# Kernel optimization log

Measured on AMD Instinct MI355X. Metric: run time of the kernel, lower is better.

The kernel has to match this reference:

```python
import jax, jax.numpy as jnp
import numpy as np
import math

INPUT_DIM, HIDDEN, OUT_DIM, NUM_LAYERS = 128, 512, 128, 2
GRID_SIZE, ORDER = 5, 3  # efficient-KAN defaults
NBASIS = GRID_SIZE + ORDER  # 8 basis functions per input feature


def _grid():
    h = 2.0 / GRID_SIZE  # grid_range [-1, 1]
    return jnp.asarray(np.arange(-ORDER, GRID_SIZE + ORDER + 1) * h - 1.0, dtype=jnp.float32)  # [12]


def b_splines(x, grid):
    # x: [B, In] -> [B, In, NBASIS] via Cox-de Boor recursion (order 3)
    x = x[..., None]
    bases = ((x >= grid[:-1]) & (x < grid[1:])).astype(x.dtype)
    for p in range(1, ORDER + 1):
        left = (x - grid[:-(p + 1)]) / (grid[p:-1] - grid[:-(p + 1)]) * bases[..., :-1]
        right = (grid[p + 1:] - x) / (grid[p + 1:] - grid[1:-p]) * bases[..., 1:]
        bases = left + right
    return bases


def kan_layer(x, base_w, spline_w, grid):
    # efficient-KAN: silu base branch + B-spline branch
    B = x.shape[0]
    out = jax.nn.silu(x) @ base_w.T
    spl = b_splines(x, grid).reshape(B, -1) @ spline_w.reshape(spline_w.shape[0], -1).T
    return out + spl


def lstm_cell(inp, h, c, w_ih, w_hh, b_ih, b_hh, kan_base, kan_spline, grid):
    gates = inp @ w_ih.T + b_ih + h @ w_hh.T + b_hh  # [B, 3H]
    i_g, f_g, o_g = jnp.split(jax.nn.sigmoid(gates), 3, axis=1)
    g = kan_layer(jnp.concatenate([inp, h], axis=1), kan_base, kan_spline, grid)
    c_next = f_g * c + i_g * g
    h_next = o_g * jnp.tanh(c_next)
    return h_next, c_next


def setup_inputs() -> dict:
    key = jax.random.key(0)
    ks = jax.random.split(key, 32)
    stdv = 1.0 / math.sqrt(HIDDEN)
    u = lambda k, shape: jax.random.uniform(k, shape, jnp.float32, -stdv, stdv)
    d = {"x": jax.random.normal(ks[0], (64, 256, INPUT_DIM), jnp.float32)}
    for L in range(NUM_LAYERS):
        In = INPUT_DIM if L == 0 else HIDDEN
        b = 8 * L
        d[f"w_ih{L}"] = u(ks[b + 1], (3 * HIDDEN, In))
        d[f"w_hh{L}"] = u(ks[b + 2], (3 * HIDDEN, HIDDEN))
        d[f"b_ih{L}"] = jnp.zeros((3 * HIDDEN,), jnp.float32)
        d[f"b_hh{L}"] = jnp.zeros((3 * HIDDEN,), jnp.float32)
        d[f"kan_base{L}"] = u(ks[b + 3], (HIDDEN, In + HIDDEN))
        d[f"kan_spline{L}"] = u(ks[b + 4], (HIDDEN, In + HIDDEN, NBASIS)) * 0.1
    d["fc_w"] = u(ks[20], (OUT_DIM, HIDDEN))
    d["fc_b"] = u(ks[21], (OUT_DIM,))
    return d


def reference(x, w_ih0, w_hh0, b_ih0, b_hh0, kan_base0, kan_spline0,
              w_ih1, w_hh1, b_ih1, b_hh1, kan_base1, kan_spline1, fc_w, fc_b):
    grid = _grid()
    B = x.shape[0]
    layers = [
        (w_ih0, w_hh0, b_ih0, b_hh0, kan_base0, kan_spline0),
        (w_ih1, w_hh1, b_ih1, b_hh1, kan_base1, kan_spline1),
    ]
    h0 = tuple(jnp.zeros((B, HIDDEN), x.dtype) for _ in range(NUM_LAYERS))
    c0 = tuple(jnp.zeros((B, HIDDEN), x.dtype) for _ in range(NUM_LAYERS))

    def step(carry, x_t):
        hs, cs = carry
        hs, cs = list(hs), list(cs)
        inp = x_t
        for L in range(NUM_LAYERS):
            w_ih, w_hh, b_ih, b_hh, kb, ksw = layers[L]
            hs[L], cs[L] = lstm_cell(inp, hs[L], cs[L], w_ih, w_hh, b_ih, b_hh, kb, ksw, grid)
            inp = hs[L]
        return (tuple(hs), tuple(cs)), None

    xs = jnp.swapaxes(x, 0, 1)  # [T, B, D]
    (hs, _), _ = jax.lax.scan(step, (h0, c0), xs)
    return hs[-1] @ fc_w.T + fc_b
```

## Files before the change

### kernel.cpp

```cpp
#include <hip/hip_runtime.h>
#include <math.h>
#include <stdint.h>

namespace {

typedef __attribute__((ext_vector_type(8))) short short8v;
typedef __attribute__((ext_vector_type(4))) float f32x4;

constexpr int TT = 256;

constexpr size_t OFF_ST = 0;
constexpr size_t OFF_P0 = 98304;
constexpr size_t OFF_P1 = 884736;
constexpr size_t OFF_WF = 1671168;
constexpr size_t OFF_FF = 11894784;
constexpr size_t WS_NEED = 12959744ull * 4;

constexpr size_t WFLO = 10223616;
constexpr size_t FFLO = 1064960;
constexpr size_t FLB1 = 409600;

__device__ __forceinline__ float sigmoidf_(float v) { return 1.0f / (1.0f + expf(-v)); }

__device__ __forceinline__ ushort bf16h(float v) {
    uint32_t u = __float_as_uint(v);
    return (ushort)((u + 0x7fffu + ((u >> 16) & 1u)) >> 16);
}
__device__ __forceinline__ float bf16f(ushort h) { return __uint_as_float(((uint32_t)h) << 16); }

__device__ __forceinline__ void bspline8(float x, float* out) {
    const float KG[12] = {-2.2f,-1.8f,-1.4f,-1.0f,-0.6f,-0.2f,
                           0.2f, 0.6f, 1.0f, 1.4f, 1.8f, 2.2f};
    float b[11];
#pragma unroll
    for (int i = 0; i < 11; ++i)
        b[i] = (x >= KG[i] && x < KG[i + 1]) ? 1.0f : 0.0f;
#pragma unroll
    for (int p = 1; p <= 3; ++p) {
#pragma unroll
        for (int i = 0; i + p < 11; ++i) {
            float l = (x - KG[i])         * (1.0f / (KG[i + p] - KG[i]));
            float r = (KG[i + p + 1] - x) * (1.0f / (KG[i + p + 1] - KG[i + 1]));
            b[i] = l * b[i] + r * b[i + 1];
        }
    }
#pragma unroll
    for (int i = 0; i < 8; ++i) out[i] = b[i];
}

__device__ __forceinline__ void putFeat(int l, int k, int b, float z,
                                        ushort* __restrict__ fe)
{
    const int NSL = l ? 16 : 10, KC = l ? 512 : 320;
    const int kh = (k >= KC) ? 1 : 0, kr = k - kh * KC;
    const int sl = kr >> 5, kg = (kr >> 3) & 3, j = kr & 7;
    const size_t cell = (size_t)((b >> 4) * 64 + (b & 15) + 16 * kg) * 8 + j;
    const size_t LB = l ? FLB1 : 0;
    const size_t slb = ((size_t)kh * NSL + sl) * 2048 + cell;
    const size_t pstep = (size_t)2 * NSL * 2048;

    auto putp = [&](int p, float v) {
        size_t idx = LB + (size_t)p * pstep + slb;
        ushort h = bf16h(v);
        fe[idx] = h;
        fe[FFLO + idx] = bf16h(v - bf16f(h));
    };
    putp(0, z);
    putp(1, z / (1.0f + expf(-z)));
    float bs[8];
    bspline8(z, bs);
#pragma unroll
    for (int r = 0; r < 8; ++r) putp(2 + r, bs[r]);
}

__global__ __launch_bounds__(256) void sentinel_kernel(float* out, float v) {
    int i = blockIdx.x * 256 + threadIdx.x;
    if (i < 8192) out[i] = v;
}

__global__ __launch_bounds__(256) void wbuild_kernel(
    ushort* __restrict__ wf,
    const float* __restrict__ w_ih0, const float* __restrict__ w_hh0,
    const float* __restrict__ kb0, const float* __restrict__ ksp0,
    const float* __restrict__ w_ih1, const float* __restrict__ w_hh1,
    const float* __restrict__ kb1, const float* __restrict__ ksp1)
{
    const int gid = blockIdx.x * 256 + threadIdx.x;
    const int s = gid >> 6, lane = gid & 63;
    int wid, sl;
    if (s < 7680) { wid = s / 10; sl = s % 10; }
    else          { wid = 768 + (s - 7680) / 16; sl = (s - 7680) % 16; }
    const int l = wid >= 768 ? 1 : 0;
    const int r2 = wid - l * 768;
    const int kh = r2 >= 384 ? 1 : 0;
    const int tile = r2 - kh * 384;
    const int IN = l ? 512 : 128, W = IN + 512, KC = W >> 1;
    const int m = lane & 15, kg = lane >> 4;
    const int k0 = kh * KC + sl * 32;
    const int kk = k0 + kg * 8;
    const int o0 = tile * 16;

    const float* w_ih = l ? w_ih1 : w_ih0;
    const float* w_hh = l ? w_hh1 : w_hh0;
    const float* kb   = l ? kb1 : kb0;
    const float* ksp  = l ? ksp1 : ksp0;

    float vv[8];
    if (tile < 96) {
        const int row = o0 + m;
#pragma unroll
        for (int j = 0; j < 8; ++j) {
            const int k = kk + j;
            vv[j] = (k0 < IN) ? w_ih[(size_t)row * IN + k]
                              : w_hh[(size_t)row * 512 + (k - IN)];
        }
    } else if (tile < 128) {
        const int row = (tile - 96) * 16 + m;
#pragma unroll
        for (int j = 0; j < 8; ++j) vv[j] = kb[(size_t)row * W + kk + j];
    } else {
        const int rr = (tile - 128) >> 5, op = ((tile - 128) & 31) * 16 + m;
#pragma unroll
        for (int j = 0; j < 8; ++j)
            vv[j] = ksp[((size_t)op * W + kk + j) * 8 + rr];
    }
    const size_t base = (size_t)s * 512 + (size_t)lane * 8;
#pragma unroll
    for (int j = 0; j < 8; ++j) {
        ushort h = bf16h(vv[j]);
        wf[base + j] = h;
        wf[WFLO + base + j] = bf16h(vv[j] - bf16f(h));
    }
}

__global__ __launch_bounds__(256) void prologue_kernel(
    const float* __restrict__ x, float* __restrict__ ws)
{
    ushort* fe = (ushort*)(ws + OFF_FF);
    const int g = blockIdx.x * 256 + threadIdx.x;
    if (g < 98304) {
        ws[OFF_ST + g] = 0.0f;
    } else if (g < 106496) {
        const int i = g - 98304, k = i & 127, b = i >> 7;
        putFeat(0, k, b, x[((size_t)b * TT) * 128 + k], fe);
    } else if (g < 139264) {
        const int i = g - 106496, o = i & 511, b = i >> 9;
        putFeat(0, 128 + o, b, 0.0f, fe);
    } else {
        const int i = g - 139264, o = i & 511, b = i >> 9;
        putFeat(1, 512 + o, b, 0.0f, fe);
    }
}

__global__ __launch_bounds__(256) void phaseA_kernel(
    float* __restrict__ ws, int s)
{
    __shared__ short8v sfh[2][256], sfl[2][256];

    const int t = threadIdx.x, lane = t & 63;
    const int wv = __builtin_amdgcn_readfirstlane(t >> 6);
    const int bid = blockIdx.x;
    const int task = ((bid & 7) * 48) + (bid >> 3);
    const int l  = task >= 192 ? 1 : 0;
    if (l ? (s < 1) : (s >= TT)) return;
    const int r3 = task - l * 192;
    const int kh = r3 >= 96 ? 1 : 0;
    const int grp = r3 - kh * 96;
    const int tile = grp * 4 + wv;
    const int NSL = l ? 16 : 10;
    const int p = (grp < 24) ? 0 : (grp < 32) ? 1 : (2 + ((grp - 32) >> 3));

    const ushort* wf = (const ushort*)(ws + OFF_WF);
    const ushort* fe = (const ushort*)(ws + OFF_FF);
    float* pout = ws + (l ? OFF_P1 : OFF_P0) + (size_t)kh * 393216;

    const int wid = l * 768 + kh * 384 + tile;
    const size_t sbase = l ? (7680 + (size_t)(wid - 768) * 16) : (size_t)wid * 10;
    const size_t fbase = (l ? FLB1 : 0) +
                         ((size_t)(p * 2 + kh) * NSL) * 2048;

    const int m = lane & 15, kg = lane >> 4;
    const int o0 = tile * 16;

    f32x4 acc[4] = {{0,0,0,0},{0,0,0,0},{0,0,0,0},{0,0,0,0}};

    {
        short8v rh = *(const short8v*)(fe + fbase + (size_t)t * 8);
        short8v rl = *(const short8v*)(fe + FFLO + fbase + (size_t)t * 8);
        sfh[0][t] = rh; sfl[0][t] = rl;
    }
    short8v cwh = *(const short8v*)(wf + sbase * 512 + (size_t)lane * 8);
    short8v cwl = *(const short8v*)(wf + WFLO + sbase * 512 + (size_t)lane * 8);
    __syncthreads();

    int cur = 0;
    for (int sl = 0; sl < NSL; ++sl) {
        const bool hasNext = (sl + 1 < NSL);
        short8v nfh, nfl, nwh, nwl;
        if (hasNext) {
            const size_t nb = fbase + (size_t)(sl + 1) * 2048 + (size_t)t * 8;
            nfh = *(const short8v*)(fe + nb);
            nfl = *(const short8v*)(fe + FFLO + nb);
            const size_t wb = (sbase + sl + 1) * 512 + (size_t)lane * 8;
            nwh = *(const short8v*)(wf + wb);
            nwl = *(const short8v*)(wf + WFLO + wb);
        }

#pragma unroll
        for (int bt = 0; bt < 4; ++bt) {
            short8v bh = sfh[cur][bt * 64 + lane];
            short8v bl = sfl[cur][bt * 64 + lane];
            acc[bt] = __builtin_amdgcn_mfma_f32_16x16x32_bf16(cwh, bh, acc[bt], 0, 0, 0);
            acc[bt] = __builtin_amdgcn_mfma_f32_16x16x32_bf16(cwh, bl, acc[bt], 0, 0, 0);
            acc[bt] = __builtin_amdgcn_mfma_f32_16x16x32_bf16(cwl, bh, acc[bt], 0, 0, 0);
        }

        if (hasNext) {
            sfh[cur ^ 1][t] = nfh;
            sfl[cur ^ 1][t] = nfl;
            cwh = nwh; cwl = nwl;
            __syncthreads();
            cur ^= 1;
        }
    }

#pragma unroll
    for (int bt = 0; bt < 4; ++bt) {
        float* dst = pout + (size_t)(bt * 16 + m) * 6144 + o0 + kg * 4;
        *(float4*)dst = (float4){acc[bt][0], acc[bt][1], acc[bt][2], acc[bt][3]};
    }
}

__global__ __launch_bounds__(256) void phaseB_kernel(
    float* __restrict__ ws,
    const float* __restrict__ b_ih0, const float* __restrict__ b_hh0,
    const float* __restrict__ b_ih1, const float* __restrict__ b_hh1,
    const float* __restrict__ x, int s)
{
    ushort* fe = (ushort*)(ws + OFF_FF);
    float* c0T = ws + OFF_ST;
    float* h1T = c0T + 32768;
    float* c1T = h1T + 32768;
    const float* p0 = ws + OFF_P0;
    const float* p1 = ws + OFF_P1;

    const int u = blockIdx.x * 256 + threadIdx.x;
    if (u < 32768) {
        if (s >= TT) return;
        const int o = u & 511, b = u >> 9;
        auto P = [&](int rw) {
            return p0[(size_t)b * 6144 + rw] + p0[393216 + (size_t)b * 6144 + rw];
        };
        float si = P(o)        + b_ih0[o]        + b_hh0[o];
        float sf = P(512 + o)  + b_ih0[512 + o]  + b_hh0[512 + o];
        float sO = P(1024 + o) + b_ih0[1024 + o] + b_hh0[1024 + o];
        float sk = P(1536 + o);
#pragma unroll
        for (int rr = 0; rr < 8; ++rr) sk += P(2048 + rr * 512 + o);
        float ig = sigmoidf_(si), fg = sigmoidf_(sf), og = sigmoidf_(sO);
        float c = fg * c0T[(size_t)b * 512 + o] + ig * sk;
        c0T[(size_t)b * 512 + o] = c;
        float z = og * tanhf(c);
        putFeat(1, o, b, z, fe);
        putFeat(0, 128 + o, b, z, fe);
    } else if (u < 65536) {
        if (s < 1) return;
        const int v = u - 32768, o = v & 511, b = v >> 9;
        auto P = [&](int rw) {
            return p1[(size_t)b * 6144 + rw] + p1[393216 + (size_t)b * 6144 + rw];
        };
        float si = P(o)        + b_ih1[o]        + b_hh1[o];
        float sf = P(512 + o)  + b_ih1[512 + o]  + b_hh1[512 + o];
        float sO = P(1024 + o) + b_ih1[1024 + o] + b_hh1[1024 + o];
        float sk = P(1536 + o);
#pragma unroll
        for (int rr = 0; rr < 8; ++rr) sk += P(2048 + rr * 512 + o);
        float ig = sigmoidf_(si), fg = sigmoidf_(sf), og = sigmoidf_(sO);
        float c = fg * c1T[(size_t)b * 512 + o] + ig * sk;
        c1T[(size_t)b * 512 + o] = c;
        float z = og * tanhf(c);
        h1T[(size_t)b * 512 + o] = z;
        putFeat(1, 512 + o, b, z, fe);
    } else {
        if (s + 1 >= TT) return;
        const int v = u - 65536, k = v & 127, b = v >> 7;
        putFeat(0, k, b, x[((size_t)b * TT + (s + 1)) * 128 + k], fe);
    }
}

__global__ __launch_bounds__(256) void final_fc(
    const float* __restrict__ h1T, const float* __restrict__ fc_w,
    const float* __restrict__ fc_b, float* __restrict__ out)
{
    const int gid = blockIdx.x * 256 + threadIdx.x;
    const int b = gid & 63, jo = gid >> 6;
    float a = fc_b[jo];
    const float* hr = h1T + (size_t)b * 512;
    const float* wr = fc_w + (size_t)jo * 512;
    for (int o = 0; o < 512; o += 4) {
        float4 h4 = *(const float4*)(hr + o);
        float4 w4 = *(const float4*)(wr + o);
        a = fmaf(h4.x, w4.x, a); a = fmaf(h4.y, w4.y, a);
        a = fmaf(h4.z, w4.z, a); a = fmaf(h4.w, w4.w, a);
    }
    out[(size_t)b * 128 + jo] = a;
}

}

extern "C" void kernel_launch(void* const* d_in, const int* in_sizes, int n_in,
                              void* d_out, int out_size, void* d_ws, size_t ws_size,
                              hipStream_t stream) {
    (void)out_size;
    float* out = (float*)d_out;

    static const int EXP_SIZES[15] = {
        64 * 256 * 128, 1536 * 128, 1536 * 512, 1536, 1536,
        512 * 640, 512 * 640 * 8,
        1536 * 512, 1536 * 512, 1536, 1536,
        512 * 1024, 512 * 1024 * 8,
        128 * 512, 128
    };
    if (n_in != 15) { sentinel_kernel<<<32, 256, 0, stream>>>(out, 111.0f); return; }
    for (int i = 0; i < 15; ++i)
        if (in_sizes[i] != EXP_SIZES[i]) {
            sentinel_kernel<<<32, 256, 0, stream>>>(out, 200.0f * (i + 1)); return;
        }
    if (ws_size < WS_NEED) { sentinel_kernel<<<32, 256, 0, stream>>>(out, 7777.0f); return; }

    const float* x     = (const float*)d_in[0];
    const float* w_ih0 = (const float*)d_in[1];
    const float* w_hh0 = (const float*)d_in[2];
    const float* b_ih0 = (const float*)d_in[3];
    const float* b_hh0 = (const float*)d_in[4];
    const float* kb0   = (const float*)d_in[5];
    const float* ksp0  = (const float*)d_in[6];
    const float* w_ih1 = (const float*)d_in[7];
    const float* w_hh1 = (const float*)d_in[8];
    const float* b_ih1 = (const float*)d_in[9];
    const float* b_hh1 = (const float*)d_in[10];
    const float* kb1   = (const float*)d_in[11];
    const float* ksp1  = (const float*)d_in[12];
    const float* fc_w  = (const float*)d_in[13];
    const float* fc_b  = (const float*)d_in[14];

    float* ws = (float*)d_ws;

    prologue_kernel<<<672, 256, 0, stream>>>(x, ws);
    wbuild_kernel<<<4992, 256, 0, stream>>>((ushort*)(ws + OFF_WF),
        w_ih0, w_hh0, kb0, ksp0, w_ih1, w_hh1, kb1, ksp1);

    for (int s = 0; s <= TT; ++s) {
        phaseA_kernel<<<384, 256, 0, stream>>>(ws, s);
        phaseB_kernel<<<288, 256, 0, stream>>>(
            ws, b_ih0, b_hh0, b_ih1, b_hh1, x, s);
    }

    final_fc<<<32, 256, 0, stream>>>(ws + OFF_ST + 32768, fc_w, fc_b, out);
}
```

Measured before the change: 5.226 ms.

## Process two K-slices per barrier and prefetch two iterations ahead in phaseA

```diff
diff --git a/kernel.cpp b/kernel.cpp
--- a/kernel.cpp
+++ b/kernel.cpp
@@ -155,7 +155,7 @@
 __global__ __launch_bounds__(256) void phaseA_kernel(
     float* __restrict__ ws, int s)
 {
-    __shared__ short8v sfh[2][256], sfl[2][256];
+    __shared__ short8v sfh[2][2][256], sfl[2][2][256];
 
     const int t = threadIdx.x, lane = t & 63;
     const int wv = __builtin_amdgcn_readfirstlane(t >> 6);
@@ -168,6 +168,7 @@
     const int grp = r3 - kh * 96;
     const int tile = grp * 4 + wv;
     const int NSL = l ? 16 : 10;
+    const int NP  = NSL >> 1;
     const int p = (grp < 24) ? 0 : (grp < 32) ? 1 : (2 + ((grp - 32) >> 3));
 
     const ushort* wf = (const ushort*)(ws + OFF_WF);
@@ -184,43 +185,73 @@
 
     f32x4 acc[4] = {{0,0,0,0},{0,0,0,0},{0,0,0,0},{0,0,0,0}};
 
-    {
-        short8v rh = *(const short8v*)(fe + fbase + (size_t)t * 8);
-        short8v rl = *(const short8v*)(fe + FFLO + fbase + (size_t)t * 8);
-        sfh[0][t] = rh; sfl[0][t] = rl;
-    }
-    short8v cwh = *(const short8v*)(wf + sbase * 512 + (size_t)lane * 8);
-    short8v cwl = *(const short8v*)(wf + WFLO + sbase * 512 + (size_t)lane * 8);
+    sfh[0][0][t] = *(const short8v*)(fe + fbase + (size_t)t * 8);
+    sfl[0][0][t] = *(const short8v*)(fe + FFLO + fbase + (size_t)t * 8);
+    sfh[0][1][t] = *(const short8v*)(fe + fbase + 2048 + (size_t)t * 8);
+    sfl[0][1][t] = *(const short8v*)(fe + FFLO + fbase + 2048 + (size_t)t * 8);
+    short8v cwh0 = *(const short8v*)(wf + (sbase + 0) * 512 + (size_t)lane * 8);
+    short8v cwl0 = *(const short8v*)(wf + WFLO + (sbase + 0) * 512 + (size_t)lane * 8);
+    short8v cwh1 = *(const short8v*)(wf + (sbase + 1) * 512 + (size_t)lane * 8);
+    short8v cwl1 = *(const short8v*)(wf + WFLO + (sbase + 1) * 512 + (size_t)lane * 8);
+
+    short8v af0h, af0l, af1h, af1l, aw0h, aw0l, aw1h, aw1l;
+    if (NP > 1) {
+        const size_t nb = fbase + 2 * 2048 + (size_t)t * 8;
+        af0h = *(const short8v*)(fe + nb);
+        af0l = *(const short8v*)(fe + FFLO + nb);
+        af1h = *(const short8v*)(fe + nb + 2048);
+        af1l = *(const short8v*)(fe + FFLO + nb + 2048);
+        const size_t wb = (sbase + 2) * 512 + (size_t)lane * 8;
+        aw0h = *(const short8v*)(wf + wb);
+        aw0l = *(const short8v*)(wf + WFLO + wb);
+        aw1h = *(const short8v*)(wf + wb + 512);
+        aw1l = *(const short8v*)(wf + WFLO + wb + 512);
+    }
     __syncthreads();
 
     int cur = 0;
-    for (int sl = 0; sl < NSL; ++sl) {
-        const bool hasNext = (sl + 1 < NSL);
-        short8v nfh, nfl, nwh, nwl;
-        if (hasNext) {
-            const size_t nb = fbase + (size_t)(sl + 1) * 2048 + (size_t)t * 8;
-            nfh = *(const short8v*)(fe + nb);
-            nfl = *(const short8v*)(fe + FFLO + nb);
-            const size_t wb = (sbase + sl + 1) * 512 + (size_t)lane * 8;
-            nwh = *(const short8v*)(wf + wb);
-            nwl = *(const short8v*)(wf + WFLO + wb);
+    for (int sp = 0; sp < NP; ++sp) {
+        short8v bf0h, bf0l, bf1h, bf1l, bw0h, bw0l, bw1h, bw1l;
+        if (sp + 2 < NP) {
+            const size_t nb = fbase + (size_t)(sp + 2) * 2 * 2048 + (size_t)t * 8;
+            bf0h = *(const short8v*)(fe + nb);
+            bf0l = *(const short8v*)(fe + FFLO + nb);
+            bf1h = *(const short8v*)(fe + nb + 2048);
+            bf1l = *(const short8v*)(fe + FFLO + nb + 2048);
+            const size_t wb = (sbase + (sp + 2) * 2) * 512 + (size_t)lane * 8;
+            bw0h = *(const short8v*)(wf + wb);
+            bw0l = *(const short8v*)(wf + WFLO + wb);
+            bw1h = *(const short8v*)(wf + wb + 512);
+            bw1l = *(const short8v*)(wf + WFLO + wb + 512);
         }
 
 #pragma unroll
         for (int bt = 0; bt < 4; ++bt) {
-            short8v bh = sfh[cur][bt * 64 + lane];
-            short8v bl = sfl[cur][bt * 64 + lane];
-            acc[bt] = __builtin_amdgcn_mfma_f32_16x16x32_bf16(cwh, bh, acc[bt], 0, 0, 0);
-            acc[bt] = __builtin_amdgcn_mfma_f32_16x16x32_bf16(cwh, bl, acc[bt], 0, 0, 0);
-            acc[bt] = __builtin_amdgcn_mfma_f32_16x16x32_bf16(cwl, bh, acc[bt], 0, 0, 0);
-        }
-
-        if (hasNext) {
-            sfh[cur ^ 1][t] = nfh;
-            sfl[cur ^ 1][t] = nfl;
-            cwh = nwh; cwl = nwl;
+            short8v bh = sfh[cur][0][bt * 64 + lane];
+            short8v bl = sfl[cur][0][bt * 64 + lane];
+            acc[bt] = __builtin_amdgcn_mfma_f32_16x16x32_bf16(cwh0, bh, acc[bt], 0, 0, 0);
+            acc[bt] = __builtin_amdgcn_mfma_f32_16x16x32_bf16(cwh0, bl, acc[bt], 0, 0, 0);
+            acc[bt] = __builtin_amdgcn_mfma_f32_16x16x32_bf16(cwl0, bh, acc[bt], 0, 0, 0);
+        }
+#pragma unroll
+        for (int bt = 0; bt < 4; ++bt) {
+            short8v bh = sfh[cur][1][bt * 64 + lane];
+            short8v bl = sfl[cur][1][bt * 64 + lane];
+            acc[bt] = __builtin_amdgcn_mfma_f32_16x16x32_bf16(cwh1, bh, acc[bt], 0, 0, 0);
+            acc[bt] = __builtin_amdgcn_mfma_f32_16x16x32_bf16(cwh1, bl, acc[bt], 0, 0, 0);
+            acc[bt] = __builtin_amdgcn_mfma_f32_16x16x32_bf16(cwl1, bh, acc[bt], 0, 0, 0);
+        }
+
+        if (sp + 1 < NP) {
+            sfh[cur ^ 1][0][t] = af0h;
+            sfl[cur ^ 1][0][t] = af0l;
+            sfh[cur ^ 1][1][t] = af1h;
+            sfl[cur ^ 1][1][t] = af1l;
+            cwh0 = aw0h; cwl0 = aw0l; cwh1 = aw1h; cwl1 = aw1l;
             __syncthreads();
             cur ^= 1;
+            af0h = bf0h; af0l = bf0l; af1h = bf1h; af1l = bf1l;
+            aw0h = bw0h; aw0l = bw0l; aw1h = bw1h; aw1l = bw1l;
         }
     }
 
```

Measured after the change: 4.750 ms (median of 2 runs). 1.1x faster.
